# Optimization experiments

Measured on AMD Instinct MI355X. Metric: run time of the kernel, lower is better.

The kernel has to match this reference:

```python
import jax, jax.numpy as jnp
import numpy as np

B, H, W, C = 64, 56, 56, 192
HEADS, WS, SHIFT, HID, DEPTH = 6, 7, 3, 768, 2
N = WS * WS
HEAD_DIM = C // HEADS
SCALE = HEAD_DIM ** -0.5


def _rel_index(ws):
    coords = np.stack(np.meshgrid(np.arange(ws), np.arange(ws), indexing='ij'))  # (2,ws,ws)
    cf = coords.reshape(2, -1)
    rel = (cf[:, :, None] - cf[:, None, :]).transpose(1, 2, 0).astype(np.int64)  # (N,N,2)
    rel[:, :, 0] += ws - 1
    rel[:, :, 1] += ws - 1
    rel[:, :, 0] *= 2 * ws - 1
    return rel.sum(-1)  # (N,N) into (2ws-1)^2 table


def _attn_mask(hh, ww, ws, ss):
    img = np.zeros((hh, ww))
    cnt = 0
    for hs in (slice(0, -ws), slice(-ws, -ss), slice(-ss, None)):
        for wsl in (slice(0, -ws), slice(-ws, -ss), slice(-ss, None)):
            img[hs, wsl] = cnt
            cnt += 1
    mw = img.reshape(hh // ws, ws, ww // ws, ws).transpose(0, 2, 1, 3).reshape(-1, ws * ws)
    diff = mw[:, None, :] - mw[:, :, None]  # (nW, N, N)
    return np.where(diff != 0, -100.0, 0.0).astype(np.float32)

REL_IDX = _rel_index(WS)                    # (N,N) static
ATTN_MASK = jnp.asarray(_attn_mask(H, W, WS, SHIFT))  # (nW,N,N) static


def _win_part(x):  # (B,H,W,C) -> (B*nW, N, C)
    b, h, w, c = x.shape
    x = x.reshape(b, h // WS, WS, w // WS, WS, c).transpose(0, 1, 3, 2, 4, 5)
    return x.reshape(-1, N, c)


def _win_rev(wins, h, w):  # (B*nW, N, C) -> (B,H,W,C)
    c = wins.shape[-1]
    b = wins.shape[0] // ((h // WS) * (w // WS))
    x = wins.reshape(b, h // WS, w // WS, WS, WS, c).transpose(0, 1, 3, 2, 4, 5)
    return x.reshape(b, h, w, c)


def _ln(x, g, b):
    mu = x.mean(-1, keepdims=True)
    var = x.var(-1, keepdims=True)
    return (x - mu) * jax.lax.rsqrt(var + 1e-5) * g + b


def setup_inputs() -> dict:
    key = jax.random.key(0)
    ks = jax.random.split(key, 8)
    s = 0.02
    return {
        'x': jax.random.normal(ks[0], (B, H * W, C), jnp.float32),
        'ln1_g': jnp.ones((DEPTH, C), jnp.float32),
        'ln1_b': jnp.zeros((DEPTH, C), jnp.float32),
        'qkv_w': jax.random.normal(ks[1], (DEPTH, C, 3 * C), jnp.float32) * s,
        'qkv_b': jnp.zeros((DEPTH, 3 * C), jnp.float32),
        'rpb': jax.random.normal(ks[2], (DEPTH, (2 * WS - 1) ** 2, HEADS), jnp.float32) * s,
        'proj_w': jax.random.normal(ks[3], (DEPTH, C, C), jnp.float32) * s,
        'proj_b': jnp.zeros((DEPTH, C), jnp.float32),
        'ln2_g': jnp.ones((DEPTH, C), jnp.float32),
        'ln2_b': jnp.zeros((DEPTH, C), jnp.float32),
        'fc1_w': jax.random.normal(ks[4], (DEPTH, C, HID), jnp.float32) * s,
        'fc1_b': jnp.zeros((DEPTH, HID), jnp.float32),
        'fc2_w': jax.random.normal(ks[5], (DEPTH, HID, C), jnp.float32) * s,
        'fc2_b': jnp.zeros((DEPTH, C), jnp.float32),
    }


def _block(x, shift, ln1g, ln1b, qw, qb, rpb_t, pw, pb, ln2g, ln2b, f1w, f1b, f2w, f2b):
    shortcut = x
    h = _ln(x, ln1g, ln1b).reshape(B, H, W, C)
    if shift > 0:
        h = jnp.roll(h, (-shift, -shift), axis=(1, 2))
    xw = _win_part(h)                                   # (B*nW, N, C)
    qkv = xw @ qw + qb                                  # (B*nW, N, 3C)
    qkv = qkv.reshape(-1, N, 3, HEADS, HEAD_DIM)
    q, k, v = qkv[:, :, 0], qkv[:, :, 1], qkv[:, :, 2]  # (B*nW, N, h, d)
    attn = jnp.einsum('wnhd,wmhd->whnm', q * SCALE, k)  # (B*nW, h, N, N)
    bias = rpb_t[REL_IDX.reshape(-1)].reshape(N, N, HEADS).transpose(2, 0, 1)
    attn = attn + bias[None]
    if shift > 0:
        nw = ATTN_MASK.shape[0]
        attn = attn.reshape(B, nw, HEADS, N, N) + ATTN_MASK[None, :, None]
        attn = attn.reshape(-1, HEADS, N, N)
    attn = jax.nn.softmax(attn, axis=-1)
    out = jnp.einsum('whnm,wmhd->wnhd', attn, v).reshape(-1, N, C)
    out = out @ pw + pb
    h = _win_rev(out, H, W)
    if shift > 0:
        h = jnp.roll(h, (shift, shift), axis=(1, 2))
    x = shortcut + h.reshape(B, H * W, C)
    y = _ln(x, ln2g, ln2b)
    y = jax.nn.gelu(y @ f1w + f1b, approximate=False) @ f2w + f2b
    return x + y


def reference(x, ln1_g, ln1_b, qkv_w, qkv_b, rpb, proj_w, proj_b,
              ln2_g, ln2_b, fc1_w, fc1_b, fc2_w, fc2_b):
    for i in range(DEPTH):
        shift = 0 if i % 2 == 0 else SHIFT
        x = _block(x, shift, ln1_g[i], ln1_b[i], qkv_w[i], qkv_b[i], rpb[i],
                   proj_w[i], proj_b[i], ln2_g[i], ln2_b[i],
                   fc1_w[i], fc1_b[i], fc2_w[i], fc2_b[i])
    return x
```

## Files before the change

### kernel.cpp

```cpp
#include <hip/hip_runtime.h>
#include <hip/hip_bf16.h>
#include <math.h>

typedef __attribute__((ext_vector_type(8))) short short8;
typedef __attribute__((ext_vector_type(4))) float floatx4;
typedef __attribute__((ext_vector_type(4))) unsigned short ushort4v;

#define SCALE_F 0.17677669529663689f

__device__ __forceinline__ float bf2f(__hip_bfloat16 v){ return __bfloat162float(v); }

__global__ void wcast_t(const float* __restrict__ src, __hip_bfloat16* __restrict__ dst, int K, int N)
{
    int idx = blockIdx.x * 256 + threadIdx.x;
    if (idx >= K * N) return;
    int n = idx / K, k = idx - n * K;
    dst[idx] = __float2bfloat16(src[(size_t)k * N + n]);
}

__global__ __launch_bounds__(256)
void ln_kernel(const float* __restrict__ x, const float* __restrict__ g,
               const float* __restrict__ bb, __hip_bfloat16* __restrict__ out, int b0)
{
    int wave = threadIdx.x >> 6, lane = threadIdx.x & 63;
    int wr = blockIdx.x * 4 + wave;
    const float* xr = x + ((size_t)b0 * 3136 + wr) * 192;
    float v0 = xr[lane], v1 = xr[lane + 64], v2 = xr[lane + 128];
    float s = v0 + v1 + v2, ss = v0 * v0 + v1 * v1 + v2 * v2;
    #pragma unroll
    for (int o = 32; o; o >>= 1) { s += __shfl_xor(s, o); ss += __shfl_xor(ss, o); }
    float mu = s * (1.f / 192.f);
    float rs = rsqrtf(ss * (1.f / 192.f) - mu * mu + 1e-5f);
    __hip_bfloat16* op = out + (size_t)wr * 192;
    op[lane]       = __float2bfloat16((v0 - mu) * rs * g[lane]       + bb[lane]);
    op[lane + 64]  = __float2bfloat16((v1 - mu) * rs * g[lane + 64]  + bb[lane + 64]);
    op[lane + 128] = __float2bfloat16((v2 - mu) * rs * g[lane + 128] + bb[lane + 128]);
}

__global__ __launch_bounds__(64)
void attn_mfma(const __hip_bfloat16* __restrict__ qkv, const float* __restrict__ rpb,
               __hip_bfloat16* __restrict__ out, int shift)
{
    __shared__ float rp_s[169];
    __shared__ __align__(16) unsigned short Ps[64 * 72];
    const int win = blockIdx.x, head = blockIdx.y;
    const int lane = threadIdx.x;
    const int q = lane >> 4, l = lane & 15;
    const int bl = win >> 6, wrem = win & 63;
    const int wh = wrem >> 3, ww = wrem & 7;
    const __hip_bfloat16* base = qkv + head * 32;

    for (int i = lane; i < 169; i += 64) rp_s[i] = rpb[i * 6 + head];

    auto tokof = [&](int m) -> int {
        int mi = (m * 37) >> 8; int mj = m - mi * 7;
        int hh = wh * 7 + mi + shift; if (hh >= 56) hh -= 56;
        int wp = ww * 7 + mj + shift; if (wp >= 56) wp -= 56;
        return bl * 3136 + hh * 56 + wp;
    };

    short8 kf[4], qf[4];
    #pragma unroll
    for (int t = 0; t < 4; ++t) {
        int m = t * 16 + l; int mc = m < 49 ? m : 48;
        int r = tokof(mc);
        kf[t] = *(const short8*)(base + (size_t)r * 576 + 192 + q * 8);
        qf[t] = *(const short8*)(base + (size_t)r * 576 + q * 8);
    }
    floatx4 st[4][4];
    #pragma unroll
    for (int mt = 0; mt < 4; ++mt)
        #pragma unroll
        for (int nt = 0; nt < 4; ++nt) {
            floatx4 z = {0.f, 0.f, 0.f, 0.f};
            st[mt][nt] = __builtin_amdgcn_mfma_f32_16x16x32_bf16(kf[mt], qf[nt], z, 0, 0, 0);
        }

    short8 vb[2][2];
    #pragma unroll
    for (int mk = 0; mk < 2; ++mk)
        #pragma unroll
        for (int j = 0; j < 8; ++j) {
            int m = mk * 32 + q * 8 + j; int mc = m < 49 ? m : 48;
            int r = tokof(mc);
            const short* vp = (const short*)(base + (size_t)r * 576 + 384 + l);
            vb[mk][0][j] = vp[0];
            vb[mk][1][j] = vp[16];
        }

    const bool edgeH = (wh == 7), edgeW = (ww == 7);
    int mi[16], mj[16], idm[16]; bool mok[16];
    #pragma unroll
    for (int mt = 0; mt < 4; ++mt)
        #pragma unroll
        for (int r = 0; r < 4; ++r) {
            int ii = mt * 4 + r;
            int m = mt * 16 + q * 4 + r;
            int d7 = (m * 37) >> 8;
            mi[ii] = d7; mj[ii] = m - d7 * 7;
            mok[ii] = (m < 49);
            int ih = edgeH ? (d7 < 4 ? 1 : 2) : 0;
            int iw = edgeW ? ((m - d7 * 7) < 4 ? 1 : 2) : 0;
            idm[ii] = ih * 3 + iw;
        }
    __syncthreads();

    #pragma unroll
    for (int nt = 0; nt < 4; ++nt) {
        int n = nt * 16 + l;
        int ri = (n * 37) >> 8; int rj = n - ri * 7;
        int ihn = edgeH ? (ri < 4 ? 1 : 2) : 0;
        int iwn = edgeW ? (rj < 4 ? 1 : 2) : 0;
        int idn = ihn * 3 + iwn;
        float sv[16];
        float mx = -3e38f;
        #pragma unroll
        for (int mt = 0; mt < 4; ++mt)
            #pragma unroll
            for (int r = 0; r < 4; ++r) {
                int ii = mt * 4 + r;
                float s = st[mt][nt][r] * SCALE_F + rp_s[(ri - mi[ii] + 6) * 13 + (rj - mj[ii] + 6)];
                if (shift > 0 && idm[ii] != idn) s -= 100.f;
                if (!mok[ii]) s = -3e38f;
                sv[ii] = s;
                mx = fmaxf(mx, s);
            }
        mx = fmaxf(mx, __shfl_xor(mx, 16));
        mx = fmaxf(mx, __shfl_xor(mx, 32));
        float sum = 0.f;
        #pragma unroll
        for (int ii = 0; ii < 16; ++ii) { float e = __expf(sv[ii] - mx); sv[ii] = e; sum += e; }
        sum += __shfl_xor(sum, 16);
        sum += __shfl_xor(sum, 32);
        float inv = 1.f / sum;
        #pragma unroll
        for (int mt = 0; mt < 4; ++mt) {
            ushort4v pk;
            #pragma unroll
            for (int r = 0; r < 4; ++r) {
                __hip_bfloat16 h = __float2bfloat16(sv[mt * 4 + r] * inv);
                pk[r] = *(unsigned short*)&h;
            }
            *(ushort4v*)(&Ps[(size_t)(nt * 16 + l) * 72 + mt * 16 + q * 4]) = pk;
        }
    }
    __syncthreads();

    floatx4 o[4][2];
    #pragma unroll
    for (int nt = 0; nt < 4; ++nt)
        #pragma unroll
        for (int dt = 0; dt < 2; ++dt) o[nt][dt] = floatx4{0.f, 0.f, 0.f, 0.f};
    #pragma unroll
    for (int mk = 0; mk < 2; ++mk)
        #pragma unroll
        for (int nt = 0; nt < 4; ++nt) {
            short8 pf = *(const short8*)(&Ps[(size_t)(nt * 16 + l) * 72 + mk * 32 + q * 8]);
            #pragma unroll
            for (int dt = 0; dt < 2; ++dt)
                o[nt][dt] = __builtin_amdgcn_mfma_f32_16x16x32_bf16(pf, vb[mk][dt], o[nt][dt], 0, 0, 0);
        }
    #pragma unroll
    for (int nt = 0; nt < 4; ++nt)
        #pragma unroll
        for (int r = 0; r < 4; ++r) {
            int n = nt * 16 + q * 4 + r;
            if (n < 49) {
                int tn = tokof(n);
                __hip_bfloat16* op = out + (size_t)tn * 192 + head * 32 + l;
                op[0]  = __float2bfloat16(o[nt][0][r]);
                op[16] = __float2bfloat16(o[nt][1][r]);
            }
        }
}

#define AST 200

__device__ __forceinline__ void stage_a192(const __hip_bfloat16* Atile, __hip_bfloat16* As, int tid)
{
    #pragma unroll
    for (int i = 0; i < 12; ++i) {
        int c = i * 256 + tid;
        int row = (c * 2731) >> 16;
        int col = c - row * 24;
        uint4 v = *(const uint4*)(Atile + (size_t)c * 8);
        *(uint4*)(As + row * AST + col * 8) = v;
    }
}

__device__ __forceinline__ void stage_b192(const __hip_bfloat16* Btile, __hip_bfloat16* Bs, int tid)
{
    #pragma unroll
    for (int i = 0; i < 6; ++i) {
        int c = i * 256 + tid;
        int row = (c * 2731) >> 16;
        int col = c - row * 24;
        uint4 v = *(const uint4*)(Btile + (size_t)c * 8);
        *(uint4*)(Bs + row * AST + col * 8) = v;
    }
}

template<int EPI, int NT>
__global__ __launch_bounds__(256)
void gemm_k192(const __hip_bfloat16* __restrict__ A,
               const __hip_bfloat16* __restrict__ Wt,
               const float* __restrict__ bias,
               __hip_bfloat16* __restrict__ out, int ld)
{
    __shared__ __align__(16) __hip_bfloat16 As[128 * AST];
    __shared__ __align__(16) __hip_bfloat16 Bs[64 * AST];
    const int tid = threadIdx.x;
    const int wave = tid >> 6, lane = tid & 63;
    const int q = lane >> 4, l = lane & 15;
    const int row0 = blockIdx.x * 128;

    stage_a192(A + (size_t)row0 * 192, As, tid);

    for (int ct = 0; ct < NT; ++ct) {
        __syncthreads();
        stage_b192(Wt + (size_t)ct * 64 * 192, Bs, tid);
        __syncthreads();
        floatx4 acc[2][4];
        #pragma unroll
        for (int rt = 0; rt < 2; ++rt)
            #pragma unroll
            for (int c = 0; c < 4; ++c) acc[rt][c] = floatx4{0.f, 0.f, 0.f, 0.f};
        #pragma unroll
        for (int k = 0; k < 6; ++k) {
            short8 a0 = *(const short8*)(As + (wave * 32 + l) * AST + k * 32 + q * 8);
            short8 a1 = *(const short8*)(As + (wave * 32 + 16 + l) * AST + k * 32 + q * 8);
            #pragma unroll
            for (int c = 0; c < 4; ++c) {
                short8 bf = *(const short8*)(Bs + (c * 16 + l) * AST + k * 32 + q * 8);
                acc[0][c] = __builtin_amdgcn_mfma_f32_16x16x32_bf16(a0, bf, acc[0][c], 0, 0, 0);
                acc[1][c] = __builtin_amdgcn_mfma_f32_16x16x32_bf16(a1, bf, acc[1][c], 0, 0, 0);
            }
        }
        #pragma unroll
        for (int c = 0; c < 4; ++c) {
            int col = ct * 64 + c * 16 + l;
            float bz = bias[col];
            #pragma unroll
            for (int rt = 0; rt < 2; ++rt)
                #pragma unroll
                for (int rr = 0; rr < 4; ++rr) {
                    int row = row0 + wave * 32 + rt * 16 + q * 4 + rr;
                    float v = acc[rt][c][rr] + bz;
                    if constexpr (EPI == 1)
                        v = 0.5f * v * (1.f + erff(v * 0.70710678118654752f));
                    out[(size_t)row * ld + col] = __float2bfloat16(v);
                }
        }
    }
}

__global__ __launch_bounds__(256)
void gemm_proj_ln(const __hip_bfloat16* __restrict__ A,
                  const __hip_bfloat16* __restrict__ Wt,
                  const float* __restrict__ pb,
                  const float* __restrict__ g2, const float* __restrict__ b2,
                  const float* __restrict__ resid, float* __restrict__ Rout,
                  __hip_bfloat16* __restrict__ lnout, int b0)
{
    __shared__ __align__(16) __hip_bfloat16 As[128 * AST];
    __shared__ __align__(16) __hip_bfloat16 Bs[64 * AST];
    const int tid = threadIdx.x;
    const int wave = tid >> 6, lane = tid & 63;
    const int q = lane >> 4, l = lane & 15;
    const int row0 = blockIdx.x * 128;

    stage_a192(A + (size_t)row0 * 192, As, tid);

    floatx4 acc[2][12];
    #pragma unroll
    for (int rt = 0; rt < 2; ++rt)
        #pragma unroll
        for (int j = 0; j < 12; ++j) acc[rt][j] = floatx4{0.f, 0.f, 0.f, 0.f};

    for (int ct = 0; ct < 3; ++ct) {
        __syncthreads();
        stage_b192(Wt + (size_t)ct * 64 * 192, Bs, tid);
        __syncthreads();
        #pragma unroll
        for (int k = 0; k < 6; ++k) {
            short8 a0 = *(const short8*)(As + (wave * 32 + l) * AST + k * 32 + q * 8);
            short8 a1 = *(const short8*)(As + (wave * 32 + 16 + l) * AST + k * 32 + q * 8);
            #pragma unroll
            for (int c = 0; c < 4; ++c) {
                short8 bf = *(const short8*)(Bs + (c * 16 + l) * AST + k * 32 + q * 8);
                acc[0][ct * 4 + c] = __builtin_amdgcn_mfma_f32_16x16x32_bf16(a0, bf, acc[0][ct * 4 + c], 0, 0, 0);
                acc[1][ct * 4 + c] = __builtin_amdgcn_mfma_f32_16x16x32_bf16(a1, bf, acc[1][ct * 4 + c], 0, 0, 0);
            }
        }
    }

    float gj[12], bj[12], pbj[12];
    #pragma unroll
    for (int j = 0; j < 12; ++j) {
        int col = (j >> 2) * 64 + (j & 3) * 16 + l;
        gj[j] = g2[col]; bj[j] = b2[col]; pbj[j] = pb[col];
    }
    #pragma unroll
    for (int rt = 0; rt < 2; ++rt)
        #pragma unroll
        for (int rr = 0; rr < 4; ++rr) {
            int row = row0 + wave * 32 + rt * 16 + q * 4 + rr;
            size_t rb = ((size_t)b0 * 3136 + row) * 192;
            float y[12];
            float s = 0.f, ss = 0.f;
            #pragma unroll
            for (int j = 0; j < 12; ++j) {
                int col = (j >> 2) * 64 + (j & 3) * 16 + l;
                float v = acc[rt][j][rr] + pbj[j] + resid[rb + col];
                y[j] = v; s += v; ss += v * v;
                Rout[rb + col] = v;
            }
            s += __shfl_xor(s, 1); ss += __shfl_xor(ss, 1);
            s += __shfl_xor(s, 2); ss += __shfl_xor(ss, 2);
            s += __shfl_xor(s, 4); ss += __shfl_xor(ss, 4);
            s += __shfl_xor(s, 8); ss += __shfl_xor(ss, 8);
            float mu = s * (1.f / 192.f);
            float rs = rsqrtf(ss * (1.f / 192.f) - mu * mu + 1e-5f);
            #pragma unroll
            for (int j = 0; j < 12; ++j) {
                int col = (j >> 2) * 64 + (j & 3) * 16 + l;
                lnout[(size_t)row * 192 + col] = __float2bfloat16((y[j] - mu) * rs * gj[j] + bj[j]);
            }
        }
}

__global__ __launch_bounds__(256)
void gemm_fc2(const __hip_bfloat16* __restrict__ A,
              const __hip_bfloat16* __restrict__ Wt,
              const float* __restrict__ bias,
              const float* __restrict__ resid, float* __restrict__ out, int b0)
{
    __shared__ __align__(16) __hip_bfloat16 As[128 * AST];
    __shared__ __align__(16) __hip_bfloat16 Bs[64 * AST];
    const int tid = threadIdx.x;
    const int wave = tid >> 6, lane = tid & 63;
    const int q = lane >> 4, l = lane & 15;
    const int row0 = blockIdx.x * 128;

    floatx4 acc[2][12];
    #pragma unroll
    for (int rt = 0; rt < 2; ++rt)
        #pragma unroll
        for (int j = 0; j < 12; ++j) acc[rt][j] = floatx4{0.f, 0.f, 0.f, 0.f};

    for (int kc = 0; kc < 4; ++kc) {
        __syncthreads();
        #pragma unroll
        for (int i = 0; i < 12; ++i) {
            int c = i * 256 + tid;
            int row = (c * 2731) >> 16;
            int col = c - row * 24;
            uint4 v = *(const uint4*)(A + (size_t)(row0 + row) * 768 + kc * 192 + col * 8);
            *(uint4*)(As + row * AST + col * 8) = v;
        }
        for (int ct = 0; ct < 3; ++ct) {
            __syncthreads();
            #pragma unroll
            for (int i = 0; i < 6; ++i) {
                int c = i * 256 + tid;
                int row = (c * 2731) >> 16;
                int col = c - row * 24;
                uint4 v = *(const uint4*)(Wt + (size_t)(ct * 64 + row) * 768 + kc * 192 + col * 8);
                *(uint4*)(Bs + row * AST + col * 8) = v;
            }
            __syncthreads();
            #pragma unroll
            for (int k = 0; k < 6; ++k) {
                short8 a0 = *(const short8*)(As + (wave * 32 + l) * AST + k * 32 + q * 8);
                short8 a1 = *(const short8*)(As + (wave * 32 + 16 + l) * AST + k * 32 + q * 8);
                #pragma unroll
                for (int c = 0; c < 4; ++c) {
                    short8 bf = *(const short8*)(Bs + (c * 16 + l) * AST + k * 32 + q * 8);
                    acc[0][ct * 4 + c] = __builtin_amdgcn_mfma_f32_16x16x32_bf16(a0, bf, acc[0][ct * 4 + c], 0, 0, 0);
                    acc[1][ct * 4 + c] = __builtin_amdgcn_mfma_f32_16x16x32_bf16(a1, bf, acc[1][ct * 4 + c], 0, 0, 0);
                }
            }
        }
    }

    float bzj[12];
    #pragma unroll
    for (int j = 0; j < 12; ++j) {
        int col = (j >> 2) * 64 + (j & 3) * 16 + l;
        bzj[j] = bias[col];
    }
    #pragma unroll
    for (int rt = 0; rt < 2; ++rt)
        #pragma unroll
        for (int rr = 0; rr < 4; ++rr) {
            int row = row0 + wave * 32 + rt * 16 + q * 4 + rr;
            size_t rb = ((size_t)b0 * 3136 + row) * 192;
            #pragma unroll
            for (int j = 0; j < 12; ++j) {
                int col = (j >> 2) * 64 + (j & 3) * 16 + l;
                out[rb + col] = resid[rb + col] + acc[rt][j][rr] + bzj[j];
            }
        }
}

extern "C" void kernel_launch(void* const* d_in, const int* in_sizes, int n_in,
                              void* d_out, int out_size, void* d_ws, size_t ws_size,
                              hipStream_t stream)
{
    const float* x      = (const float*)d_in[0];
    const float* ln1_g  = (const float*)d_in[1];
    const float* ln1_b  = (const float*)d_in[2];
    const float* qkv_w  = (const float*)d_in[3];
    const float* qkv_b  = (const float*)d_in[4];
    const float* rpb    = (const float*)d_in[5];
    const float* proj_w = (const float*)d_in[6];
    const float* proj_b = (const float*)d_in[7];
    const float* ln2_g  = (const float*)d_in[8];
    const float* ln2_b  = (const float*)d_in[9];
    const float* fc1_w  = (const float*)d_in[10];
    const float* fc1_b  = (const float*)d_in[11];
    const float* fc2_w  = (const float*)d_in[12];
    const float* fc2_b  = (const float*)d_in[13];

    char* ws = (char*)d_ws;
    const size_t RN = 200704ull;

    int CB = 64;
    auto need = [&](int cb) -> size_t {
        return RN * 192 * 4
             + (size_t)cb * 3136 * (192 + 768 + 192) * 2
             + 884736ull * 2 + 4096;
    };
    while (CB > 2 && need(CB) > ws_size) CB >>= 1;

    float* R = (float*)ws;
    size_t off = RN * 192 * 4;
    __hip_bfloat16* bufA = (__hip_bfloat16*)(ws + off); off += (size_t)CB * 3136 * 192 * 2;
    __hip_bfloat16* bufB = (__hip_bfloat16*)(ws + off); off += (size_t)CB * 3136 * 768 * 2;
    __hip_bfloat16* bufC = (__hip_bfloat16*)(ws + off); off += (size_t)CB * 3136 * 192 * 2;
    __hip_bfloat16* wreg = (__hip_bfloat16*)(ws + off);

    __hip_bfloat16 *qkvWt[2], *projWt[2], *fc1Wt[2], *fc2Wt[2];
    size_t woff = 0;
    for (int d = 0; d < 2; ++d) { qkvWt[d] = wreg + woff; woff += 576 * 192; }
    for (int d = 0; d < 2; ++d) { projWt[d] = wreg + woff; woff += 192 * 192; }
    for (int d = 0; d < 2; ++d) { fc1Wt[d] = wreg + woff; woff += 768 * 192; }
    for (int d = 0; d < 2; ++d) { fc2Wt[d] = wreg + woff; woff += 192 * 768; }

    for (int d = 0; d < 2; ++d) {
        wcast_t<<<(192 * 576 + 255) / 256, 256, 0, stream>>>(qkv_w + (size_t)d * 192 * 576, qkvWt[d], 192, 576);
        wcast_t<<<(192 * 192 + 255) / 256, 256, 0, stream>>>(proj_w + (size_t)d * 192 * 192, projWt[d], 192, 192);
        wcast_t<<<(192 * 768 + 255) / 256, 256, 0, stream>>>(fc1_w + (size_t)d * 192 * 768, fc1Wt[d], 192, 768);
        wcast_t<<<(768 * 192 + 255) / 256, 256, 0, stream>>>(fc2_w + (size_t)d * 768 * 192, fc2Wt[d], 768, 192);
    }

    const int nrows = CB * 3136;
    const int gm = nrows / 128;
    for (int d = 0; d < 2; ++d) {
        int shift = d ? 3 : 0;
        const float* residA = d ? R : x;
        const float* rpbd = rpb + (size_t)d * 169 * 6;
        float* outF = d ? (float*)d_out : R;

        for (int b0 = 0; b0 < 64; b0 += CB) {
            ln_kernel<<<nrows / 4, 256, 0, stream>>>(residA, ln1_g + d * 192, ln1_b + d * 192, bufA, b0);
            gemm_k192<0, 9><<<gm, 256, 0, stream>>>(bufA, qkvWt[d], qkv_b + d * 576, bufB, 576);
            attn_mfma<<<dim3(CB * 64, 6), 64, 0, stream>>>(bufB, rpbd, bufA, shift);
            gemm_proj_ln<<<gm, 256, 0, stream>>>(bufA, projWt[d], proj_b + d * 192,
                                                 ln2_g + d * 192, ln2_b + d * 192,
                                                 residA, R, bufC, b0);
            gemm_k192<1, 12><<<gm, 256, 0, stream>>>(bufC, fc1Wt[d], fc1_b + d * 768, bufB, 768);
            gemm_fc2<<<gm, 256, 0, stream>>>(bufB, fc2Wt[d], fc2_b + d * 192, R, outF, b0);
        }
    }
}
```

Baseline: 2.081 ms.

## Double-buffer weight tiles via async global-to-LDS loads in K=192 GEMM

The K=192 GEMM now keeps the whole A row-block in registers instead of staging it in LDS. Weight tiles are prefetched with global_load_lds into a double-buffered, XOR-swizzled LDS array, so the next tile loads while the current one is being multiplied. Waves are rearranged into a 2x2 grid with 4x2 MFMA tiles each, which raises reuse of each B fragment. This costs more VGPRs for the A fragments, adds launch_bounds occupancy 3, and relies on manual vmcnt waits and barriers being correct.

Measured after the change: 2.642 ms. 1.27x slower.

```diff
diff --git a/kernel.cpp b/kernel.cpp
--- a/kernel.cpp
+++ b/kernel.cpp
@@ -200,51 +200,94 @@
     }
 }
 
+__device__ __forceinline__ void stage_b_async(const __hip_bfloat16* __restrict__ Wtile,
+                                              void* BsBuf, const int* srcoff, int wave)
+{
+    const char* src = (const char*)Wtile;
+    char* dst = (char*)BsBuf + wave * 6144;
+    #pragma unroll
+    for (int j = 0; j < 6; ++j) {
+        __builtin_amdgcn_global_load_lds(
+            (const __attribute__((address_space(1))) void*)(src + srcoff[j]),
+            (__attribute__((address_space(3))) void*)(dst + j * 1024),
+            16, 0, 0);
+    }
+}
+
 template<int EPI, int NT>
-__global__ __launch_bounds__(256)
+__global__ __launch_bounds__(256, 3)
 void gemm_k192(const __hip_bfloat16* __restrict__ A,
                const __hip_bfloat16* __restrict__ Wt,
                const float* __restrict__ bias,
                __hip_bfloat16* __restrict__ out, int ld)
 {
-    __shared__ __align__(16) __hip_bfloat16 As[128 * AST];
-    __shared__ __align__(16) __hip_bfloat16 Bs[64 * AST];
+    __shared__ __align__(16) unsigned short Bs[2][64 * 192];
     const int tid = threadIdx.x;
     const int wave = tid >> 6, lane = tid & 63;
     const int q = lane >> 4, l = lane & 15;
+    const int wr = wave >> 1, wc = wave & 1;
     const int row0 = blockIdx.x * 128;
 
-    stage_a192(A + (size_t)row0 * 192, As, tid);
+    short8 af[4][6];
+    const __hip_bfloat16* abase = A + (size_t)(row0 + wr * 64 + l) * 192 + q * 8;
+    #pragma unroll
+    for (int rt = 0; rt < 4; ++rt)
+        #pragma unroll
+        for (int k = 0; k < 6; ++k)
+            af[rt][k] = *(const short8*)(abase + (size_t)rt * 16 * 192 + k * 32);
+
+    int srcoff[6];
+    #pragma unroll
+    for (int j = 0; j < 6; ++j) {
+        int g = (wave * 6 + j) * 64 + lane;
+        int d = g * 16;
+        int row = d / 384;
+        srcoff[j] = d ^ ((row & 7) << 4);
+    }
+
+    const int sw2 = (q * 16) ^ ((l & 7) << 4);
+
+    stage_b_async(Wt, &Bs[0][0], srcoff, wave);
 
     for (int ct = 0; ct < NT; ++ct) {
-        __syncthreads();
-        stage_b192(Wt + (size_t)ct * 64 * 192, Bs, tid);
-        __syncthreads();
-        floatx4 acc[2][4];
-        #pragma unroll
-        for (int rt = 0; rt < 2; ++rt)
-            #pragma unroll
-            for (int c = 0; c < 4; ++c) acc[rt][c] = floatx4{0.f, 0.f, 0.f, 0.f};
+        if (ct + 1 < NT)
+            stage_b_async(Wt + (size_t)(ct + 1) * 64 * 192, &Bs[(ct + 1) & 1][0], srcoff, wave);
+        asm volatile("s_waitcnt vmcnt(6)" ::: "memory");
+        __builtin_amdgcn_s_barrier();
+        asm volatile("" ::: "memory");
+
+        const char* bsb = (const char*)&Bs[ct & 1][0];
+        floatx4 acc[4][2];
+        #pragma unroll
+        for (int rt = 0; rt < 4; ++rt)
+            #pragma unroll
+            for (int c = 0; c < 2; ++c) acc[rt][c] = floatx4{0.f, 0.f, 0.f, 0.f};
+
         #pragma unroll
         for (int k = 0; k < 6; ++k) {
-            short8 a0 = *(const short8*)(As + (wave * 32 + l) * AST + k * 32 + q * 8);
-            short8 a1 = *(const short8*)(As + (wave * 32 + 16 + l) * AST + k * 32 + q * 8);
-            #pragma unroll
-            for (int c = 0; c < 4; ++c) {
-                short8 bf = *(const short8*)(Bs + (c * 16 + l) * AST + k * 32 + q * 8);
-                acc[0][c] = __builtin_amdgcn_mfma_f32_16x16x32_bf16(a0, bf, acc[0][c], 0, 0, 0);
-                acc[1][c] = __builtin_amdgcn_mfma_f32_16x16x32_bf16(a1, bf, acc[1][c], 0, 0, 0);
-            }
-        }
-        #pragma unroll
-        for (int c = 0; c < 4; ++c) {
-            int col = ct * 64 + c * 16 + l;
+            #pragma unroll
+            for (int c = 0; c < 2; ++c) {
+                const char* pc = bsb + ((wc * 2 + c) * 16 + l) * 384;
+                short8 bf = *(const short8*)(pc + ((k * 64) ^ sw2));
+                #pragma unroll
+                for (int rt = 0; rt < 4; ++rt)
+                    acc[rt][c] = __builtin_amdgcn_mfma_f32_16x16x32_bf16(af[rt][k], bf, acc[rt][c], 0, 0, 0);
+            }
+        }
+
+        asm volatile("" ::: "memory");
+        __builtin_amdgcn_s_barrier();
+        asm volatile("" ::: "memory");
+
+        #pragma unroll
+        for (int c = 0; c < 2; ++c) {
+            int col = ct * 64 + wc * 32 + c * 16 + l;
             float bz = bias[col];
             #pragma unroll
-            for (int rt = 0; rt < 2; ++rt)
+            for (int rt = 0; rt < 4; ++rt)
                 #pragma unroll
                 for (int rr = 0; rr < 4; ++rr) {
-                    int row = row0 + wave * 32 + rt * 16 + q * 4 + rr;
+                    int row = row0 + wr * 64 + rt * 16 + q * 4 + rr;
                     float v = acc[rt][c][rr] + bz;
                     if constexpr (EPI == 1)
                         v = 0.5f * v * (1.f + erff(v * 0.70710678118654752f));
```
